# Kernel tuning notes

Measured on AMD Instinct MI355X. Metric: run time of the kernel, lower is better.

Reference implementation:

```python
import jax, jax.numpy as jnp
import numpy as np

NUM_HEADS = 16
NUM_KV_HEADS = 2
HEAD_DIM = 256
HIDDEN = 2048
ROT_DIM = 64          # head_dim * partial_rotary_factor (0.25)
ROPE_THETA = 10000.0
EPS = 1e-6
T = 4096


def setup_inputs() -> dict:
    key = jax.random.key(0)
    k1, k2, k3, k4, k5 = jax.random.split(key, 5)
    qkv_out = HEAD_DIM * (NUM_HEADS * 2 + 2 * NUM_KV_HEADS)  # 9216 (q+gate, k, v)
    return {
        "hidden_states": jax.random.normal(k1, (T, HIDDEN), dtype=jnp.float32),
        "positions": jnp.arange(T, dtype=jnp.int32),
        "w_qkv": jax.random.normal(k2, (HIDDEN, qkv_out), dtype=jnp.float32) * 0.02,
        "w_o": jax.random.normal(k3, (NUM_HEADS * HEAD_DIM, HIDDEN), dtype=jnp.float32) * 0.02,
        "q_norm_w": jax.random.normal(k4, (HEAD_DIM,), dtype=jnp.float32) * 0.1,
        "k_norm_w": jax.random.normal(k5, (HEAD_DIM,), dtype=jnp.float32) * 0.1,
    }


def _gemma_rmsnorm(x, w):
    # GemmaRMSNorm: fp32 compute, scale by (1 + weight)
    xf = x.astype(jnp.float32)
    xf = xf * jax.lax.rsqrt(jnp.mean(xf * xf, axis=-1, keepdims=True) + EPS)
    return (xf * (1.0 + w.astype(jnp.float32))).astype(x.dtype)


def _apply_rope(x, positions):
    # neox-style partial RoPE on first ROT_DIM dims; x: [T, H, D]
    half = ROT_DIM // 2
    inv_freq = 1.0 / (ROPE_THETA ** (jnp.arange(0, ROT_DIM, 2, dtype=jnp.float32) / ROT_DIM))
    freqs = positions.astype(jnp.float32)[:, None] * inv_freq  # [T, half]
    cos = jnp.cos(freqs)[:, None, :]  # [T, 1, half]
    sin = jnp.sin(freqs)[:, None, :]
    x1 = x[..., :half]
    x2 = x[..., half:ROT_DIM]
    rot = jnp.concatenate([x1 * cos - x2 * sin, x2 * cos + x1 * sin], axis=-1)
    return jnp.concatenate([rot, x[..., ROT_DIM:]], axis=-1)


def reference(hidden_states, positions, w_qkv, w_o, q_norm_w, k_norm_w):
    q_size = NUM_HEADS * HEAD_DIM
    kv_size = NUM_KV_HEADS * HEAD_DIM
    qkv = hidden_states @ w_qkv  # [T, 2*q_size + 2*kv_size]

    # split q+gate (interleaved per head), k, v
    q_gate = qkv[:, : 2 * q_size].reshape(-1, NUM_HEADS, 2 * HEAD_DIM)
    q = q_gate[..., :HEAD_DIM]          # [T, H, D]
    gate = q_gate[..., HEAD_DIM:]       # [T, H, D]
    k = qkv[:, 2 * q_size : 2 * q_size + kv_size].reshape(-1, NUM_KV_HEADS, HEAD_DIM)
    v = qkv[:, 2 * q_size + kv_size :].reshape(-1, NUM_KV_HEADS, HEAD_DIM)

    # per-head QK RMSNorm then partial RoPE
    q = _apply_rope(_gemma_rmsnorm(q, q_norm_w), positions)
    k = _apply_rope(_gemma_rmsnorm(k, k_norm_w), positions)

    # GQA causal attention
    rep = NUM_HEADS // NUM_KV_HEADS
    k_rep = jnp.repeat(k, rep, axis=1)  # [T, H, D]
    v_rep = jnp.repeat(v, rep, axis=1)
    scaling = HEAD_DIM ** -0.5
    scores = jnp.einsum("qhd,khd->hqk", q, k_rep) * scaling  # [H, T, T]
    causal = positions[:, None] >= positions[None, :]
    scores = jnp.where(causal[None, :, :], scores, jnp.finfo(scores.dtype).min)
    probs = jax.nn.softmax(scores, axis=-1)
    attn = jnp.einsum("hqk,khd->qhd", probs, v_rep)  # [T, H, D]

    # sigmoid-gated output, then O projection
    attn = attn * jax.nn.sigmoid(gate)
    return attn.reshape(-1, NUM_HEADS * HEAD_DIM) @ w_o
```

## Files before the change

kernel.cpp:

```cpp
#include <hip/hip_runtime.h>

typedef __attribute__((ext_vector_type(4))) float f32x4;
typedef __attribute__((ext_vector_type(8))) __bf16 bf16x8;
typedef unsigned short ushort_t;
typedef unsigned int uint_t;
typedef __attribute__((ext_vector_type(4))) uint_t u32x4;

__device__ __forceinline__ float bf2f(ushort_t u) {
  union { uint_t i; float f; } v; v.i = ((uint_t)u) << 16; return v.f;
}
__device__ __forceinline__ ushort_t f2bf(float f) {
  union { float f; uint_t i; } v; v.f = f;
  uint_t x = v.i;
  return (ushort_t)((x + 0x7fffu + ((x >> 16) & 1u)) >> 16);
}

__device__ __forceinline__ void gload_lds16(const void* g, void* l) {
  __builtin_amdgcn_global_load_lds(
      (const __attribute__((address_space(1))) void*)g,
      (__attribute__((address_space(3))) void*)l, 16, 0, 0);
}

__global__ __launch_bounds__(256) void cast_bf16_kernel(
    const float* __restrict__ in, ushort_t* __restrict__ out, int n8) {
  int i = blockIdx.x * 256 + threadIdx.x;
  if (i >= n8) return;
  float4 a = ((const float4*)in)[i * 2];
  float4 b = ((const float4*)in)[i * 2 + 1];
  ushort4 o0 = make_ushort4(f2bf(a.x), f2bf(a.y), f2bf(a.z), f2bf(a.w));
  ushort4 o1 = make_ushort4(f2bf(b.x), f2bf(b.y), f2bf(b.z), f2bf(b.w));
  ((ushort4*)out)[i * 2] = o0;
  ((ushort4*)out)[i * 2 + 1] = o1;
}

__global__ __launch_bounds__(256) void transpose_cast_kernel(
    const float* __restrict__ in, ushort_t* __restrict__ out, int R, int C) {
  __shared__ float tile[32][33];
  int tx = threadIdx.x, ty = threadIdx.y;
  int c0 = blockIdx.x * 32, r0 = blockIdx.y * 32;
#pragma unroll
  for (int i = 0; i < 4; ++i)
    tile[ty + i * 8][tx] = in[(size_t)(r0 + ty + i * 8) * C + c0 + tx];
  __syncthreads();
#pragma unroll
  for (int i = 0; i < 4; ++i)
    out[(size_t)(c0 + ty + i * 8) * R + r0 + tx] = f2bf(tile[tx][ty + i * 8]);
}

template <int OUT_BF16>
__global__ __launch_bounds__(256, 2) void gemm_bt_kernel(
    const ushort_t* __restrict__ A, const ushort_t* __restrict__ BT,
    void* __restrict__ Cout, int M, int N, int K) {
  __shared__ ushort_t As[128 * 32];
  __shared__ ushort_t Bs[128 * 32];
  const int tid = threadIdx.x;
  const int lane = tid & 63;
  const int wid = tid >> 6;
  const int wr = wid >> 1, wc = wid & 1;
  const int qr = lane & 15, kg = lane >> 4;
  const size_t arow = (size_t)blockIdx.y * 128;
  const size_t brow = (size_t)blockIdx.x * 128;

  f32x4 acc[4][4] = {};

  for (int k0 = 0; k0 < K; k0 += 32) {
    __syncthreads();
#pragma unroll
    for (int t = 0; t < 2; ++t) {
      int c = (t * 4 + wid) * 64 + lane;
      int r = c >> 2, kc = (c & 3) * 8;
      gload_lds16(A + (arow + r) * K + k0 + kc, &As[(t * 4 + wid) * 512]);
      gload_lds16(BT + (brow + r) * K + k0 + kc, &Bs[(t * 4 + wid) * 512]);
    }
    __syncthreads();
    bf16x8 af[4], bfr[4];
#pragma unroll
    for (int m = 0; m < 4; ++m)
      af[m] = *(const bf16x8*)&As[(wr * 64 + m * 16 + qr) * 32 + kg * 8];
#pragma unroll
    for (int n = 0; n < 4; ++n)
      bfr[n] = *(const bf16x8*)&Bs[(wc * 64 + n * 16 + qr) * 32 + kg * 8];
#pragma unroll
    for (int m = 0; m < 4; ++m)
#pragma unroll
      for (int n = 0; n < 4; ++n)
        acc[m][n] = __builtin_amdgcn_mfma_f32_16x16x32_bf16(af[m], bfr[n], acc[m][n], 0, 0, 0);
  }

#pragma unroll
  for (int m = 0; m < 4; ++m)
#pragma unroll
    for (int n = 0; n < 4; ++n)
#pragma unroll
      for (int j = 0; j < 4; ++j) {
        size_t row = arow + wr * 64 + m * 16 + kg * 4 + j;
        size_t col = brow + wc * 64 + n * 16 + qr;
        float v = acc[m][n][j];
        if (OUT_BF16) ((ushort_t*)Cout)[row * N + col] = f2bf(v);
        else ((float*)Cout)[row * N + col] = v;
      }
}

__global__ __launch_bounds__(256) void normrope_kernel(
    ushort_t* __restrict__ qkv, const int* __restrict__ positions,
    const float* __restrict__ qw, const float* __restrict__ kw) {
  const int wv = blockIdx.x * 4 + (threadIdx.x >> 6);
  const int lane = threadIdx.x & 63;
  const int t = wv / 18;
  const int idx = wv % 18;
  size_t base;
  const float* w;
  if (idx < 16) { base = (size_t)t * 9216 + idx * 512; w = qw; }
  else { base = (size_t)t * 9216 + 8192 + (size_t)(idx - 16) * 256; w = kw; }

  ushort4 raw = *(const ushort4*)(qkv + base + lane * 4);
  float x0 = bf2f(raw.x), x1 = bf2f(raw.y), x2 = bf2f(raw.z), x3 = bf2f(raw.w);
  float ss = x0 * x0 + x1 * x1 + x2 * x2 + x3 * x3;
#pragma unroll
  for (int off = 1; off < 64; off <<= 1) ss += __shfl_xor(ss, off);
  float inv = rsqrtf(ss * (1.0f / 256.0f) + 1e-6f);
  const int d0 = lane * 4;
  float xn[4] = { x0 * inv * (1.f + w[d0]), x1 * inv * (1.f + w[d0 + 1]),
                  x2 * inv * (1.f + w[d0 + 2]), x3 * inv * (1.f + w[d0 + 3]) };
  float pn[4];
#pragma unroll
  for (int j = 0; j < 4; ++j) pn[j] = __shfl_xor(xn[j], 8);
  if (lane < 16) {
    const float pos = (float)positions[t];
#pragma unroll
    for (int j = 0; j < 4; ++j) {
      int d = d0 + j;
      int i = d & 31;
      float invf = __expf(-(float)i * 0.28782313662425574f);
      float fr = pos * invf;
      float s, c;
      sincosf(fr, &s, &c);
      xn[j] = (d < 32) ? (xn[j] * c - pn[j] * s) : (xn[j] * c + pn[j] * s);
    }
  }
  ushort4 o = make_ushort4(f2bf(xn[0]), f2bf(xn[1]), f2bf(xn[2]), f2bf(xn[3]));
  *(ushort4*)(qkv + base + lane * 4) = o;
}

__global__ __launch_bounds__(256, 2) void attn_kernel(
    const ushort_t* __restrict__ qkv, ushort_t* __restrict__ A2) {
  const int id = blockIdx.x;
  const int kvh = id & 1;
  const int j2 = id >> 1;
  const int qt = 63 - (j2 >> 3);
  const int h = kvh * 8 + (j2 & 7);
  const int tid = threadIdx.x;
  const int lane = tid & 63;
  const int wid = tid >> 6;
  const int qr = lane & 15, kg = lane >> 4;

  __shared__ __align__(16) ushort_t Ks[2][32 * 256];
  __shared__ __align__(16) ushort_t Vt[2][256 * 32];
  __shared__ __align__(16) ushort_t Ps[4][16 * 40];

  const int q0 = qt * 64;
  const int myq0 = q0 + wid * 16;

  bf16x8 qf[8];
#pragma unroll
  for (int kd = 0; kd < 8; ++kd)
    qf[kd] = *(const bf16x8*)(qkv + (size_t)(myq0 + qr) * 9216 + h * 512 + kd * 32 + kg * 8);

  f32x4 o[16] = {};
  float mrun[4], lrun[4];
#pragma unroll
  for (int j = 0; j < 4; ++j) { mrun[j] = -1e30f; lrun[j] = 0.f; }

  const int nt = qt * 2 + 2;

  u32x4 vlo0, vhi0, vlo1, vhi1;
  const int vr = tid & 15;
  const int vd0 = (tid >> 4) * 8;
  const int vd1 = vd0 + 128;

#pragma unroll
  for (int t = 0; t < 4; ++t) {
    int c = (t * 4 + wid) * 64 + lane;
    int r = c >> 5, dc = c & 31;
    int dcs = dc ^ (r & 7);
    gload_lds16(qkv + (size_t)r * 9216 + 8192 + kvh * 256 + dcs * 8,
                &Ks[0][(t * 4 + wid) * 512]);
  }
  {
    const ushort_t* g0 = qkv + (size_t)vr * 9216 + 8704 + kvh * 256;
    vlo0 = *(const u32x4*)(g0 + vd0);
    vhi0 = *(const u32x4*)(g0 + 16 * 9216 + vd0);
    vlo1 = *(const u32x4*)(g0 + vd1);
    vhi1 = *(const u32x4*)(g0 + 16 * 9216 + vd1);
  }

  int buf = 0;
  for (int kt = 0; kt < nt; ++kt) {
    const int kv0 = kt * 32;

    {
      char* vbase = (char*)&Vt[buf][0];
#pragma unroll
      for (int half = 0; half < 2; ++half) {
        u32x4 lo = half ? vlo1 : vlo0;
        u32x4 hi = half ? vhi1 : vhi0;
        int dbase = half ? vd1 : vd0;
#pragma unroll
        for (int w = 0; w < 4; ++w) {
          uint_t v0 = (lo[w] & 0xffffu) | (hi[w] << 16);
          uint_t v1 = (lo[w] >> 16) | (hi[w] & 0xffff0000u);
          int d0v = dbase + 2 * w, d1v = d0v + 1;
          int rsw = ((vr >> 2) * 16) + (vr & 3) * 4;
          *(uint_t*)(vbase + (d0v ^ ((d0v >> 3) & 1)) * 64 +
                     (rsw ^ ((d0v & 3) * 16))) = v0;
          *(uint_t*)(vbase + (d1v ^ ((d1v >> 3) & 1)) * 64 +
                     (rsw ^ ((d1v & 3) * 16))) = v1;
        }
      }
    }
    __syncthreads();

    if (kt + 1 < nt) {
      const int kv0n = kv0 + 32;
#pragma unroll
      for (int t = 0; t < 4; ++t) {
        int c = (t * 4 + wid) * 64 + lane;
        int r = c >> 5, dc = c & 31;
        int dcs = dc ^ (r & 7);
        gload_lds16(qkv + (size_t)(kv0n + r) * 9216 + 8192 + kvh * 256 + dcs * 8,
                    &Ks[buf ^ 1][(t * 4 + wid) * 512]);
      }
      const ushort_t* g0 = qkv + (size_t)(kv0n + vr) * 9216 + 8704 + kvh * 256;
      vlo0 = *(const u32x4*)(g0 + vd0);
      vhi0 = *(const u32x4*)(g0 + 16 * 9216 + vd0);
      vlo1 = *(const u32x4*)(g0 + vd1);
      vhi1 = *(const u32x4*)(g0 + 16 * 9216 + vd1);
    }
    __builtin_amdgcn_sched_barrier(0);

    const bool active = (kv0 <= myq0 + 15);
    if (active) {
      const ushort_t* ksb = &Ks[buf][0];
      f32x4 s0 = {0.f, 0.f, 0.f, 0.f}, s1 = {0.f, 0.f, 0.f, 0.f};
#pragma unroll
      for (int kd = 0; kd < 8; ++kd) {
        int off0 = qr * 512 + ((kd * 64 + kg * 16) ^ ((qr & 7) << 4));
        bf16x8 kf0 = *(const bf16x8*)((const char*)ksb + off0);
        s0 = __builtin_amdgcn_mfma_f32_16x16x32_bf16(qf[kd], kf0, s0, 0, 0, 0);
        int kvr1 = 16 + qr;
        int off1 = kvr1 * 512 + ((kd * 64 + kg * 16) ^ ((kvr1 & 7) << 4));
        bf16x8 kf1 = *(const bf16x8*)((const char*)ksb + off1);
        s1 = __builtin_amdgcn_mfma_f32_16x16x32_bf16(qf[kd], kf1, s1, 0, 0, 0);
      }
#pragma unroll
      for (int j = 0; j < 4; ++j) {
        int qg = myq0 + kg * 4 + j;
        float v0 = s0[j] * 0.0625f, v1 = s1[j] * 0.0625f;
        if (kv0 + qr > qg) v0 = -1e30f;
        if (kv0 + 16 + qr > qg) v1 = -1e30f;
        float tm = fmaxf(v0, v1);
#pragma unroll
        for (int off = 1; off < 16; off <<= 1) tm = fmaxf(tm, __shfl_xor(tm, off));
        float mref;
        if (__all(tm - mrun[j] <= 8.0f)) {
          mref = mrun[j];
        } else {
          float mnew = fmaxf(mrun[j], tm);
          float corr = __expf(mrun[j] - mnew);
          lrun[j] *= corr;
#pragma unroll
          for (int n = 0; n < 16; ++n) o[n][j] *= corr;
          mrun[j] = mnew;
          mref = mnew;
        }
        float p0 = __expf(v0 - mref), p1 = __expf(v1 - mref);
        float ps = p0 + p1;
#pragma unroll
        for (int off = 1; off < 16; off <<= 1) ps += __shfl_xor(ps, off);
        lrun[j] += ps;
        *(uint_t*)((char*)&Ps[wid][0] + (kg * 4 + j) * 80 + qr * 4) =
            (uint_t)f2bf(p0) | ((uint_t)f2bf(p1) << 16);
      }
      asm volatile("" ::: "memory");
      bf16x8 pf = *(const bf16x8*)&Ps[wid][qr * 40 + kg * 8];
      const char* vtb = (const char*)&Vt[buf][0];
#pragma unroll
      for (int n = 0; n < 16; ++n) {
        int dcol = n * 16 + qr;
        int dsw = dcol ^ ((dcol >> 3) & 1);
        bf16x8 vf = *(const bf16x8*)(vtb + dsw * 64 + ((kg ^ (dcol & 3)) * 16));
        o[n] = __builtin_amdgcn_mfma_f32_16x16x32_bf16(pf, vf, o[n], 0, 0, 0);
      }
    }
    buf ^= 1;
  }

#pragma unroll
  for (int n = 0; n < 16; ++n) {
    int d = n * 16 + qr;
#pragma unroll
    for (int j = 0; j < 4; ++j) {
      int t = myq0 + kg * 4 + j;
      float val = o[n][j] / lrun[j];
      float g2 = bf2f(qkv[(size_t)t * 9216 + h * 512 + 256 + d]);
      val *= 1.0f / (1.0f + __expf(-g2));
      A2[(size_t)t * 4096 + h * 256 + d] = f2bf(val);
    }
  }
}

extern "C" void kernel_launch(void* const* d_in, const int* in_sizes, int n_in,
                              void* d_out, int out_size, void* d_ws, size_t ws_size,
                              hipStream_t stream) {
  const float* hidden = (const float*)d_in[0];
  const int* positions = (const int*)d_in[1];
  const float* w_qkv = (const float*)d_in[2];
  const float* w_o = (const float*)d_in[3];
  const float* q_norm_w = (const float*)d_in[4];
  const float* k_norm_w = (const float*)d_in[5];

  char* ws = (char*)d_ws;
  ushort_t* hb    = (ushort_t*)ws;
  ushort_t* wqkvT = (ushort_t*)(ws + 16777216);
  ushort_t* woT   = (ushort_t*)(ws + 54525952);
  ushort_t* qkvb  = (ushort_t*)(ws + 71303168);
  ushort_t* A2    = (ushort_t*)(ws + 146800640);

  hipLaunchKernelGGL(cast_bf16_kernel, dim3(4096), dim3(256), 0, stream,
                     hidden, hb, 1048576);
  hipLaunchKernelGGL(transpose_cast_kernel, dim3(288, 64), dim3(32, 8), 0, stream,
                     w_qkv, wqkvT, 2048, 9216);
  hipLaunchKernelGGL(transpose_cast_kernel, dim3(64, 128), dim3(32, 8), 0, stream,
                     w_o, woT, 4096, 2048);
  hipLaunchKernelGGL((gemm_bt_kernel<1>), dim3(72, 32), dim3(256), 0, stream,
                     hb, wqkvT, (void*)qkvb, 4096, 9216, 2048);
  hipLaunchKernelGGL(normrope_kernel, dim3(18432), dim3(256), 0, stream,
                     qkvb, positions, q_norm_w, k_norm_w);
  hipLaunchKernelGGL(attn_kernel, dim3(1024), dim3(256), 0, stream,
                     qkvb, A2);
  hipLaunchKernelGGL((gemm_bt_kernel<0>), dim3(16, 32), dim3(256), 0, stream,
                     A2, woT, d_out, 4096, 2048, 4096);
}
```

Baseline: 728.7 us.

## Double attention query tile per wave, transpose score MFMAs, swizzle GEMM blocks

The attention kernel now gives each wave 32 query rows (128 per block), so every K and V fragment read from LDS feeds two MFMAs. The score MFMA operands are swapped so probabilities come out already in the register layout the PV MFMA needs, which removes the LDS round-trip for P and cuts the row-reduction shuffles. Fully unmasked tiles skip the causal masking, MFMA sections are bracketed with s_setprio, and query tiles are paired across the grid for load balance. Both GEMMs switch to a 1D grid with an XCD-aware block swizzle to improve L2 reuse. In exchange, the doubled accumulators raise register pressure, and the grid is halved to 512 attention blocks.

```diff
diff --git a/kernel.cpp b/kernel.cpp
--- a/kernel.cpp
+++ b/kernel.cpp
@@ -50,7 +50,11 @@
 template <int OUT_BF16>
 __global__ __launch_bounds__(256, 2) void gemm_bt_kernel(
     const ushort_t* __restrict__ A, const ushort_t* __restrict__ BT,
-    void* __restrict__ Cout, int M, int N, int K) {
+    void* __restrict__ Cout, int M, int N, int K, int nx, int cpx) {
+  const int lin = blockIdx.x;
+  const int swz = (lin & 7) * cpx + (lin >> 3);
+  const int bx = swz % nx, by = swz / nx;
+
   __shared__ ushort_t As[128 * 32];
   __shared__ ushort_t Bs[128 * 32];
   const int tid = threadIdx.x;
@@ -58,8 +62,8 @@
   const int wid = tid >> 6;
   const int wr = wid >> 1, wc = wid & 1;
   const int qr = lane & 15, kg = lane >> 4;
-  const size_t arow = (size_t)blockIdx.y * 128;
-  const size_t brow = (size_t)blockIdx.x * 128;
+  const size_t arow = (size_t)by * 128;
+  const size_t brow = (size_t)bx * 128;
 
   f32x4 acc[4][4] = {};
 
@@ -142,13 +146,67 @@
   *(ushort4*)(qkv + base + lane * 4) = o;
 }
 
+__device__ __forceinline__ bf16x8 softmax_group(
+    f32x4 sA, f32x4 sB, int kv0, int qg, bool full,
+    float& mr, float& lr, f32x4* o, int kg) {
+  float v[8];
+#pragma unroll
+  for (int j = 0; j < 4; ++j) v[j] = sA[j] * 0.0625f;
+#pragma unroll
+  for (int j = 0; j < 4; ++j) v[4 + j] = sB[j] * 0.0625f;
+  if (!full) {
+#pragma unroll
+    for (int j = 0; j < 4; ++j) {
+      if (kv0 + kg * 4 + j > qg) v[j] = -1e30f;
+      if (kv0 + 16 + kg * 4 + j > qg) v[4 + j] = -1e30f;
+    }
+  }
+  float tm = v[0];
+#pragma unroll
+  for (int j = 1; j < 8; ++j) tm = fmaxf(tm, v[j]);
+  tm = fmaxf(tm, __shfl_xor(tm, 16));
+  tm = fmaxf(tm, __shfl_xor(tm, 32));
+  float mref;
+  if (__all(tm - mr <= 8.0f)) {
+    mref = mr;
+  } else {
+    float mnew = fmaxf(mr, tm);
+    float corr = __expf(mr - mnew);
+    lr *= corr;
+    float c0 = __shfl(corr, kg * 4 + 0);
+    float c1 = __shfl(corr, kg * 4 + 1);
+    float c2 = __shfl(corr, kg * 4 + 2);
+    float c3 = __shfl(corr, kg * 4 + 3);
+#pragma unroll
+    for (int n = 0; n < 16; ++n) {
+      o[n][0] *= c0; o[n][1] *= c1; o[n][2] *= c2; o[n][3] *= c3;
+    }
+    mr = mnew; mref = mnew;
+  }
+  float p[8];
+#pragma unroll
+  for (int j = 0; j < 8; ++j) p[j] = __expf(v[j] - mref);
+  float ps = 0.f;
+#pragma unroll
+  for (int j = 0; j < 8; ++j) ps += p[j];
+  ps += __shfl_xor(ps, 16);
+  ps += __shfl_xor(ps, 32);
+  lr += ps;
+  union { u32x4 u; bf16x8 b; } pk;
+#pragma unroll
+  for (int u2 = 0; u2 < 4; ++u2)
+    pk.u[u2] = (uint_t)f2bf(p[u2]) | ((uint_t)f2bf(p[4 + u2]) << 16);
+  return pk.b;
+}
+
 __global__ __launch_bounds__(256, 2) void attn_kernel(
     const ushort_t* __restrict__ qkv, ushort_t* __restrict__ A2) {
   const int id = blockIdx.x;
-  const int kvh = id & 1;
-  const int j2 = id >> 1;
-  const int qt = 63 - (j2 >> 3);
-  const int h = kvh * 8 + (j2 & 7);
+  const int g8 = id & 255, k8 = id >> 8;
+  const int t8 = g8 >> 4;
+  const int h = ((g8 & 1) << 3) | ((g8 >> 1) & 7);
+  const int qt = k8 ? (15 - t8) : (16 + t8);
+  const int kvh = g8 & 1;
   const int tid = threadIdx.x;
   const int lane = tid & 63;
   const int wid = tid >> 6;
@@ -156,22 +214,22 @@
 
   __shared__ __align__(16) ushort_t Ks[2][32 * 256];
   __shared__ __align__(16) ushort_t Vt[2][256 * 32];
-  __shared__ __align__(16) ushort_t Ps[4][16 * 40];
-
-  const int q0 = qt * 64;
-  const int myq0 = q0 + wid * 16;
-
-  bf16x8 qf[8];
-#pragma unroll
-  for (int kd = 0; kd < 8; ++kd)
-    qf[kd] = *(const bf16x8*)(qkv + (size_t)(myq0 + qr) * 9216 + h * 512 + kd * 32 + kg * 8);
-
-  f32x4 o[16] = {};
-  float mrun[4], lrun[4];
-#pragma unroll
-  for (int j = 0; j < 4; ++j) { mrun[j] = -1e30f; lrun[j] = 0.f; }
-
-  const int nt = qt * 2 + 2;
+
+  const int q0 = qt * 128;
+  const int myq0 = q0 + wid * 32;
+
+  bf16x8 qf[2][8];
+#pragma unroll
+  for (int g = 0; g < 2; ++g)
+#pragma unroll
+    for (int kd = 0; kd < 8; ++kd)
+      qf[g][kd] = *(const bf16x8*)(qkv + (size_t)(myq0 + g * 16 + qr) * 9216 +
+                                   h * 512 + kd * 32 + kg * 8);
+
+  f32x4 o0[16] = {}, o1[16] = {};
+  float mr0 = -1e30f, mr1 = -1e30f, lr0 = 0.f, lr1 = 0.f;
+
+  const int nt = qt * 4 + 4;
 
   u32x4 vlo0, vhi0, vlo1, vhi1;
   const int vr = tid & 15;
@@ -238,73 +296,70 @@
     }
     __builtin_amdgcn_sched_barrier(0);
 
-    const bool active = (kv0 <= myq0 + 15);
+    const bool active = (kv0 <= myq0 + 31);
     if (active) {
-      const ushort_t* ksb = &Ks[buf][0];
-      f32x4 s0 = {0.f, 0.f, 0.f, 0.f}, s1 = {0.f, 0.f, 0.f, 0.f};
+      const char* ksb = (const char*)&Ks[buf][0];
+      const int kxor = (qr & 7) << 4;
+      const int kbase = qr * 512;
+      f32x4 s00 = {0.f, 0.f, 0.f, 0.f}, s01 = {0.f, 0.f, 0.f, 0.f};
+      f32x4 s10 = {0.f, 0.f, 0.f, 0.f}, s11 = {0.f, 0.f, 0.f, 0.f};
+      __builtin_amdgcn_s_setprio(1);
 #pragma unroll
       for (int kd = 0; kd < 8; ++kd) {
-        int off0 = qr * 512 + ((kd * 64 + kg * 16) ^ ((qr & 7) << 4));
-        bf16x8 kf0 = *(const bf16x8*)((const char*)ksb + off0);
-        s0 = __builtin_amdgcn_mfma_f32_16x16x32_bf16(qf[kd], kf0, s0, 0, 0, 0);
-        int kvr1 = 16 + qr;
-        int off1 = kvr1 * 512 + ((kd * 64 + kg * 16) ^ ((kvr1 & 7) << 4));
-        bf16x8 kf1 = *(const bf16x8*)((const char*)ksb + off1);
-        s1 = __builtin_amdgcn_mfma_f32_16x16x32_bf16(qf[kd], kf1, s1, 0, 0, 0);
-      }
-#pragma unroll
-      for (int j = 0; j < 4; ++j) {
-        int qg = myq0 + kg * 4 + j;
-        float v0 = s0[j] * 0.0625f, v1 = s1[j] * 0.0625f;
-        if (kv0 + qr > qg) v0 = -1e30f;
-        if (kv0 + 16 + qr > qg) v1 = -1e30f;
-        float tm = fmaxf(v0, v1);
-#pragma unroll
-        for (int off = 1; off < 16; off <<= 1) tm = fmaxf(tm, __shfl_xor(tm, off));
-        float mref;
-        if (__all(tm - mrun[j] <= 8.0f)) {
-          mref = mrun[j];
-        } else {
-          float mnew = fmaxf(mrun[j], tm);
-          float corr = __expf(mrun[j] - mnew);
-          lrun[j] *= corr;
-#pragma unroll
-          for (int n = 0; n < 16; ++n) o[n][j] *= corr;
-          mrun[j] = mnew;
-          mref = mnew;
-        }
-        float p0 = __expf(v0 - mref), p1 = __expf(v1 - mref);
-        float ps = p0 + p1;
-#pragma unroll
-        for (int off = 1; off < 16; off <<= 1) ps += __shfl_xor(ps, off);
-        lrun[j] += ps;
-        *(uint_t*)((char*)&Ps[wid][0] + (kg * 4 + j) * 80 + qr * 4) =
-            (uint_t)f2bf(p0) | ((uint_t)f2bf(p1) << 16);
-      }
-      asm volatile("" ::: "memory");
-      bf16x8 pf = *(const bf16x8*)&Ps[wid][qr * 40 + kg * 8];
+        int off = kbase + ((kd * 64 + kg * 16) ^ kxor);
+        bf16x8 kf0 = *(const bf16x8*)(ksb + off);
+        bf16x8 kf1 = *(const bf16x8*)(ksb + off + 8192);
+        s00 = __builtin_amdgcn_mfma_f32_16x16x32_bf16(kf0, qf[0][kd], s00, 0, 0, 0);
+        s01 = __builtin_amdgcn_mfma_f32_16x16x32_bf16(kf0, qf[1][kd], s01, 0, 0, 0);
+        s10 = __builtin_amdgcn_mfma_f32_16x16x32_bf16(kf1, qf[0][kd], s10, 0, 0, 0);
+        s11 = __builtin_amdgcn_mfma_f32_16x16x32_bf16(kf1, qf[1][kd], s11, 0, 0, 0);
+      }
+      __builtin_amdgcn_s_setprio(0);
+
+      const bool full = (kv0 + 31 <= myq0);
+      bf16x8 pf0 = softmax_group(s00, s10, kv0, myq0 + qr, full, mr0, lr0, o0, kg);
+      bf16x8 pf1 = softmax_group(s01, s11, kv0, myq0 + 16 + qr, full, mr1, lr1, o1, kg);
+
       const char* vtb = (const char*)&Vt[buf][0];
+      __builtin_amdgcn_s_setprio(1);
 #pragma unroll
       for (int n = 0; n < 16; ++n) {
         int dcol = n * 16 + qr;
         int dsw = dcol ^ ((dcol >> 3) & 1);
         bf16x8 vf = *(const bf16x8*)(vtb + dsw * 64 + ((kg ^ (dcol & 3)) * 16));
-        o[n] = __builtin_amdgcn_mfma_f32_16x16x32_bf16(pf, vf, o[n], 0, 0, 0);
-      }
+        o0[n] = __builtin_amdgcn_mfma_f32_16x16x32_bf16(pf0, vf, o0[n], 0, 0, 0);
+        o1[n] = __builtin_amdgcn_mfma_f32_16x16x32_bf16(pf1, vf, o1[n], 0, 0, 0);
+      }
+      __builtin_amdgcn_s_setprio(0);
     }
     buf ^= 1;
   }
 
+  float rl0[4], rl1[4];
+#pragma unroll
+  for (int j = 0; j < 4; ++j) {
+    rl0[j] = 1.0f / __shfl(lr0, kg * 4 + j);
+    rl1[j] = 1.0f / __shfl(lr1, kg * 4 + j);
+  }
 #pragma unroll
   for (int n = 0; n < 16; ++n) {
     int d = n * 16 + qr;
 #pragma unroll
     for (int j = 0; j < 4; ++j) {
-      int t = myq0 + kg * 4 + j;
-      float val = o[n][j] / lrun[j];
-      float g2 = bf2f(qkv[(size_t)t * 9216 + h * 512 + 256 + d]);
-      val *= 1.0f / (1.0f + __expf(-g2));
-      A2[(size_t)t * 4096 + h * 256 + d] = f2bf(val);
+      {
+        int t = myq0 + kg * 4 + j;
+        float val = o0[n][j] * rl0[j];
+        float g2 = bf2f(qkv[(size_t)t * 9216 + h * 512 + 256 + d]);
+        val *= 1.0f / (1.0f + __expf(-g2));
+        A2[(size_t)t * 4096 + h * 256 + d] = f2bf(val);
+      }
+      {
+        int t = myq0 + 16 + kg * 4 + j;
+        float val = o1[n][j] * rl1[j];
+        float g2 = bf2f(qkv[(size_t)t * 9216 + h * 512 + 256 + d]);
+        val *= 1.0f / (1.0f + __expf(-g2));
+        A2[(size_t)t * 4096 + h * 256 + d] = f2bf(val);
+      }
     }
   }
 }
@@ -332,12 +387,12 @@
                      w_qkv, wqkvT, 2048, 9216);
   hipLaunchKernelGGL(transpose_cast_kernel, dim3(64, 128), dim3(32, 8), 0, stream,
                      w_o, woT, 4096, 2048);
-  hipLaunchKernelGGL((gemm_bt_kernel<1>), dim3(72, 32), dim3(256), 0, stream,
-                     hb, wqkvT, (void*)qkvb, 4096, 9216, 2048);
+  hipLaunchKernelGGL((gemm_bt_kernel<1>), dim3(2304), dim3(256), 0, stream,
+                     hb, wqkvT, (void*)qkvb, 4096, 9216, 2048, 72, 288);
   hipLaunchKernelGGL(normrope_kernel, dim3(18432), dim3(256), 0, stream,
                      qkvb, positions, q_norm_w, k_norm_w);
-  hipLaunchKernelGGL(attn_kernel, dim3(1024), dim3(256), 0, stream,
+  hipLaunchKernelGGL(attn_kernel, dim3(512), dim3(256), 0, stream,
                      qkvb, A2);
-  hipLaunchKernelGGL((gemm_bt_kernel<0>), dim3(16, 32), dim3(256), 0, stream,
-                     A2, woT, d_out, 4096, 2048, 4096);
-}
+  hipLaunchKernelGGL((gemm_bt_kernel<0>), dim3(512), dim3(256), 0, stream,
+                     A2, woT, d_out, 4096, 2048, 4096, 16, 64);
+}
```

Measured after the change: 1.473 ms. 2.02x slower.
